# Kernel optimization log

Measured on AMD Instinct MI355X. Metric: run time of the kernel, lower is better.

Reference implementation:

```python
import jax, jax.numpy as jnp
import numpy as np

B, N, E, EMB, IN = 8192, 100, 1600, 5, 1
MLP_IN = 50 * 2 * EMB + 50 * 52  # 3100


def _glorot(k, shape):
    fan_in = shape[0]
    return (jax.random.normal(k, shape, jnp.float32) / np.sqrt(fan_in)).astype(jnp.float32)


def setup_inputs() -> dict:
    key = jax.random.key(0)
    ks = jax.random.split(key, 32)
    inp = {
        "data": jax.random.normal(ks[0], (B, N, IN), jnp.float32),
        "d": jax.random.normal(ks[1], (B, 50, 52), jnp.float32),
        "src": jax.random.randint(ks[2], (E,), 0, N, jnp.int32),
        "dst": jax.random.randint(ks[3], (E,), 0, N, jnp.int32),
    }
    # 3 GatedRGCN layers: (1->5), (5->5), (5->5); each has a feature linear W,b and a gate linear G,gb
    dims = [(IN, EMB), (EMB, EMB), (EMB, EMB)]
    for i, (fi, fo) in enumerate(dims):
        inp[f"W{i}"] = _glorot(ks[4 + 4 * i], (fi, fo))
        inp[f"b{i}"] = jnp.zeros((fo,), jnp.float32)
        inp[f"G{i}"] = _glorot(ks[5 + 4 * i], (fo, fo))
        inp[f"gb{i}"] = jnp.zeros((fo,), jnp.float32)
    # MLP head: 3100 -> 128 -> 128 -> 64 -> 2
    mdims = [(MLP_IN, 128), (128, 128), (128, 64), (64, 2)]
    for i, (fi, fo) in enumerate(mdims):
        inp[f"F{i + 1}"] = _glorot(ks[16 + 2 * i], (fi, fo))
        inp[f"fb{i + 1}"] = jnp.zeros((fo,), jnp.float32)
    return inp


def _gated_rgcn_layer(h, src, dst, W, b, G, gb):
    # h: [B, N, F_in]; sum-aggregate neighbor features along edges, then gated linear.
    msgs = h[:, src, :]                                   # [B, E, F_in] gather
    agg = jnp.zeros_like(h).at[:, dst, :].add(msgs)       # [B, N, F_in] scatter-add
    h2 = agg @ W + b                                      # [B, N, F_out]
    gate = jax.nn.sigmoid(h2 @ G + gb)                    # elementwise edge-free gate
    return jax.nn.leaky_relu(gate * h2)                   # LeakyReLU(0.01), torch default


def reference(data, d, src, dst,
              W0, b0, G0, gb0, W1, b1, G1, gb1, W2, b2, G2, gb2,
              F1, fb1, F2, fb2, F3, fb3, F4, fb4):
    x = data
    x = _gated_rgcn_layer(x, src, dst, W0, b0, G0, gb0)
    x = _gated_rgcn_layer(x, src, dst, W1, b1, G1, gb1)
    x = _gated_rgcn_layer(x, src, dst, W2, b2, G2, gb2)
    x = x.reshape(x.shape[0], -1)                         # [B, 500]
    x = jnp.concatenate([x, d.reshape(d.shape[0], -1)], axis=1)  # [B, 3100]
    x = jax.nn.leaky_relu(x @ F1 + fb1)
    x = jax.nn.leaky_relu(x @ F2 + fb2)
    x = jax.nn.leaky_relu(x @ F3 + fb3)
    x = jax.nn.sigmoid(x @ F4 + fb4)                      # [B, 2]
    return x
```

## Files before the change

kernel.cpp:

```cpp
#include <hip/hip_runtime.h>
#include <math.h>

#define NT 256
#define NTG 1024
constexpr int B_   = 8192;
constexpr int N_   = 100;
constexpr int E_   = 1600;
constexpr int EMB  = 5;
constexpr int XDIM = 500;
constexpr int DDIM = 2600;
constexpr int XWP  = 512;
constexpr int DOFF = 512;
constexpr int KPAD = 3136;
constexpr int NKC  = 98;
constexpr int H1 = 128, H2 = 128, H3 = 64, HO = 2;

typedef short short8 __attribute__((ext_vector_type(8)));
typedef float f32x4  __attribute__((ext_vector_type(4)));

__device__ __forceinline__ float leaky(float v) { return v > 0.f ? v : 0.01f * v; }
__device__ __forceinline__ float sigm(float v)  { return 1.f / (1.f + __expf(-v)); }
__device__ __forceinline__ unsigned short f2bf(float f) {
  unsigned int x = __float_as_uint(f);
  return (unsigned short)((x + 0x7fffu + ((x >> 16) & 1u)) >> 16);
}


constexpr int NDT = 6;

__global__ __launch_bounds__(NT) void setup_kernel(
    const int* __restrict__ src, const int* __restrict__ dst,
    int* __restrict__ off_g, int* __restrict__ lst_g,
    const float* __restrict__ F1, const float* __restrict__ F2, const float* __restrict__ F3,
    unsigned short* __restrict__ F1c, unsigned short* __restrict__ F2T, unsigned short* __restrict__ F3T,
    const float* __restrict__ dmat, unsigned short* __restrict__ awf)
{
  const int blk = blockIdx.x;
  const int t   = threadIdx.x;

  if (blk == 0) {
    __shared__ int cnt[N_ + 1];
    __shared__ int cur[N_];
    if (t <= N_) cnt[t] = 0;
    __syncthreads();
    for (int e = t; e < E_; e += NT) atomicAdd(&cnt[dst[e] + 1], 1);
    __syncthreads();
    if (t == 0) {
      int s = 0;
      for (int n = 0; n <= N_; ++n) { s += cnt[n]; cnt[n] = s; }
    }
    __syncthreads();
    if (t < N_) cur[t] = cnt[t];
    if (t <= N_) off_g[t] = cnt[t];
    __syncthreads();
    for (int e = t; e < E_; e += NT) {
      int d = dst[e];
      int p = atomicAdd(&cur[d], 1);
      lst_g[p] = src[e];
    }
  } else if (blk <= 320) {
    const int b = blk - 1;
    if (b < 128) {
      for (int k = t; k < KPAD; k += NT) {
        float v = 0.f;
        if (k < XDIM)                          v = F1[(size_t)k * H1 + b];
        else if (k >= DOFF && k < DOFF + DDIM) v = F1[(size_t)(k - DOFF + XDIM) * H1 + b];
        int kc = k >> 5, q = (k >> 3) & 3, e = k & 7;
        int lane = (b & 15) + q * 16;
        F1c[((size_t)(b >> 4) * NKC + kc) * 512 + lane * 8 + e] = f2bf(v);
      }
    } else if (b < 256) {
      int n = b - 128;
      if (t < 128) F2T[n * 128 + t] = f2bf(F2[(size_t)t * H2 + n]);
    } else {
      int n = b - 256;
      if (n < 64 && t < 128) F3T[n * 128 + t] = f2bf(F3[(size_t)t * H3 + n]);
    }
  } else {
    const int idx = blk - 321;
    const int R   = idx / NDT;
    const int ct  = idx - R * NDT;
    __shared__ __attribute__((aligned(16))) unsigned short tile[16][520];
    const float* dbase = dmat + (size_t)R * 16 * DDIM + ct * 512;

    if (ct < 5) {
      for (int i = t; i < 16 * 128; i += NT) {
        int r = i >> 7, c4 = i & 127;
        float4 f = *(const float4*)(dbase + (size_t)r * DDIM + c4 * 4);
        unsigned short* tp = &tile[r][c4 * 4];
        tp[0] = (unsigned short)(__float_as_uint(f.x) >> 16);
        tp[1] = (unsigned short)(__float_as_uint(f.y) >> 16);
        tp[2] = (unsigned short)(__float_as_uint(f.z) >> 16);
        tp[3] = (unsigned short)(__float_as_uint(f.w) >> 16);
      }
      __syncthreads();
      for (int i = t; i < 16 * 64; i += NT) {
        int kcL = i >> 6, lane = i & 63;
        int r = lane & 15, q = lane >> 4;
        uint4 p = *(const uint4*)&tile[r][kcL * 32 + q * 8];
        ((uint4*)awf)[((size_t)R * NKC + 16 + ct * 16 + kcL) * 64 + lane] = p;
      }
    } else {
      for (int i = t; i < 16 * 520; i += NT) ((unsigned short*)tile)[i] = 0;
      __syncthreads();
      for (int i = t; i < 16 * 10; i += NT) {
        int r = i / 10, c4 = i - r * 10;
        float4 f = *(const float4*)(dbase + (size_t)r * DDIM + c4 * 4);
        unsigned short* tp = &tile[r][c4 * 4];
        tp[0] = (unsigned short)(__float_as_uint(f.x) >> 16);
        tp[1] = (unsigned short)(__float_as_uint(f.y) >> 16);
        tp[2] = (unsigned short)(__float_as_uint(f.z) >> 16);
        tp[3] = (unsigned short)(__float_as_uint(f.w) >> 16);
      }
      __syncthreads();
      for (int i = t; i < 2 * 64; i += NT) {
        int kcL = i >> 6, lane = i & 63;
        int r = lane & 15, q = lane >> 4;
        uint4 p = *(const uint4*)&tile[r][kcL * 32 + q * 8];
        ((uint4*)awf)[((size_t)R * NKC + 96 + kcL) * 64 + lane] = p;
      }
    }
  }
}

constexpr int BT2 = 32;

__device__ __forceinline__ void rgcn_layer(
    const float* __restrict__ RB, float* __restrict__ WB,
    const float* __restrict__ wts, const int* __restrict__ soff,
    const int* __restrict__ sl160, int t, int wof)
{
  if (t < N_ * (BT2 / 4)) {
    const int n  = t >> 3;
    const int b4 = (t & 7) * 4;
    f32x4 a[5];
#pragma unroll
    for (int j = 0; j < 5; ++j) a[j] = (f32x4){0.f, 0.f, 0.f, 0.f};
    const int qe = soff[n + 1];
    for (int q = soff[n]; q < qe; ++q) {
      const float* base = RB + sl160[q] + b4;
#pragma unroll
      for (int j = 0; j < 5; ++j) a[j] += *(const f32x4*)(base + j * 32);
    }
    f32x4 h2[5];
#pragma unroll
    for (int j = 0; j < 5; ++j) {
      float bb = wts[wof + 25 + j];
      f32x4 v = (f32x4){bb, bb, bb, bb};
#pragma unroll
      for (int k = 0; k < 5; ++k) v += a[k] * wts[wof + k * 5 + j];
      h2[j] = v;
    }
#pragma unroll
    for (int j = 0; j < 5; ++j) {
      float gb = wts[wof + 55 + j];
      f32x4 g = (f32x4){gb, gb, gb, gb};
#pragma unroll
      for (int k = 0; k < 5; ++k) g += h2[k] * wts[wof + 30 + k * 5 + j];
      f32x4 o;
#pragma unroll
      for (int c = 0; c < 4; ++c) o[c] = leaky(sigm(g[c]) * h2[j][c]);
      *(f32x4*)(WB + n * 160 + j * 32 + b4) = o;
    }
  }
}

__global__ __launch_bounds__(NTG) void gnn_kernel(
    const float* __restrict__ data,
    const int* __restrict__ off_g, const int* __restrict__ lst_g,
    const float* __restrict__ W0, const float* __restrict__ b0, const float* __restrict__ G0, const float* __restrict__ gb0,
    const float* __restrict__ W1, const float* __restrict__ b1, const float* __restrict__ G1, const float* __restrict__ gb1,
    const float* __restrict__ W2, const float* __restrict__ b2, const float* __restrict__ G2, const float* __restrict__ gb2,
    unsigned short* __restrict__ awf)
{
  __shared__ __attribute__((aligned(16))) float bufA[BT2 * 513];
  __shared__ __attribute__((aligned(16))) float bufB[XDIM * BT2];
  __shared__ int   soff[N_ + 1];
  __shared__ int   sl160[E_];
  __shared__ float wts[160];
  const int t   = threadIdx.x;
  const int b0_ = blockIdx.x * BT2;

  for (int i = t; i < E_; i += NTG) sl160[i] = lst_g[i] * 160;
  if (t <= N_) soff[t] = off_g[t];
  if (t < 5)  { wts[t] = W0[t]; wts[5 + t] = b0[t]; wts[35 + t] = gb0[t]; }
  if (t < 25) { wts[10 + t] = G0[t];
                wts[40 + t] = W1[t]; wts[70 + t]  = G1[t];
                wts[100 + t] = W2[t]; wts[130 + t] = G2[t]; }
  if (t < 5)  { wts[65 + t] = b1[t]; wts[95 + t]  = gb1[t];
                wts[125 + t] = b2[t]; wts[155 + t] = gb2[t]; }
  for (int i = t; i < N_ * BT2; i += NTG) {
    int b = i / N_, n = i - b * N_;
    bufA[n * 160 + b] = data[(size_t)b0_ * N_ + i];
  }
  __syncthreads();

  if (t < N_ * (BT2 / 4)) {
    const int n  = t >> 3;
    const int b4 = (t & 7) * 4;
    f32x4 a = (f32x4){0.f, 0.f, 0.f, 0.f};
    const int qe = soff[n + 1];
    for (int q = soff[n]; q < qe; ++q) a += *(const f32x4*)(bufA + sl160[q] + b4);
    f32x4 h2[5];
#pragma unroll
    for (int j = 0; j < 5; ++j) {
      float bb = wts[5 + j];
      h2[j] = a * wts[j] + (f32x4){bb, bb, bb, bb};
    }
#pragma unroll
    for (int j = 0; j < 5; ++j) {
      float gb = wts[35 + j];
      f32x4 g = (f32x4){gb, gb, gb, gb};
#pragma unroll
      for (int k = 0; k < 5; ++k) g += h2[k] * wts[10 + k * 5 + j];
      f32x4 o;
#pragma unroll
      for (int c = 0; c < 4; ++c) o[c] = leaky(sigm(g[c]) * h2[j][c]);
      *(f32x4*)(bufB + n * 160 + j * 32 + b4) = o;
    }
  }
  __syncthreads();

  rgcn_layer(bufB, bufA, wts, soff, sl160, t, 40);
  __syncthreads();
  rgcn_layer(bufA, bufB, wts, soff, sl160, t, 100);
  __syncthreads();

  for (int i = t; i < BT2 * XWP; i += NTG) {
    int b = i & 31, r = i >> 5;
    bufA[b * 513 + r] = (r < XDIM) ? bufB[r * 32 + b] : 0.f;
  }
  __syncthreads();

  {
    const int R0 = blockIdx.x * 2;
    for (int i = t; i < 32 * 64; i += NTG) {
      int f = i >> 6, lane = i & 63;
      int h = f >> 4, kc = f & 15;
      int b = h * 16 + (lane & 15);
      int k0 = kc * 32 + (lane >> 4) * 8;
      const float* sp = bufA + b * 513 + k0;
      uint4 p;
      p.x = (unsigned)f2bf(sp[0]) | ((unsigned)f2bf(sp[1]) << 16);
      p.y = (unsigned)f2bf(sp[2]) | ((unsigned)f2bf(sp[3]) << 16);
      p.z = (unsigned)f2bf(sp[4]) | ((unsigned)f2bf(sp[5]) << 16);
      p.w = (unsigned)f2bf(sp[6]) | ((unsigned)f2bf(sp[7]) << 16);
      ((uint4*)awf)[((size_t)(R0 + h) * NKC + kc) * 64 + lane] = p;
    }
  }
}

constexpr int MBG = 32;
constexpr int MB2 = 16;
constexpr int EST = 136;
constexpr int KSPLIT = 7;
constexpr int SCC = 7;

__global__ __launch_bounds__(NT, 4) void mlp_main(
    const unsigned short* __restrict__ awf,
    const unsigned short* __restrict__ F1c, float* __restrict__ part)
{
  const int t     = threadIdx.x;
  const int rb    = blockIdx.x & 255;
  const int split = blockIdx.x >> 8;
  const int row0  = rb * MBG;
  const int lane  = t & 63;
  const int w     = t >> 6;
  const int quad  = lane >> 4;
  const int ln    = lane & 15;
  const int kc0   = split * (2 * SCC);

  const unsigned short* a0p = awf + (((size_t)(rb * 2 + 0) * NKC + kc0) * 64 + lane) * 8;
  const unsigned short* a1p = awf + (((size_t)(rb * 2 + 1) * NKC + kc0) * 64 + lane) * 8;
  const unsigned short* b0p = F1c + (((size_t)(w * 2 + 0) * NKC + kc0) * 64 + lane) * 8;
  const unsigned short* b1p = F1c + (((size_t)(w * 2 + 1) * NKC + kc0) * 64 + lane) * 8;

#define LOADF(Ax, Bx, c)                                                       \
  {                                                                            \
    _Pragma("unroll")                                                          \
    for (int s_ = 0; s_ < 2; ++s_) {                                           \
      const int o_ = (2 * (c) + s_) * 512;                                     \
      Ax[s_][0] = *(const short8*)(a0p + o_);                                  \
      Ax[s_][1] = *(const short8*)(a1p + o_);                                  \
      Bx[s_][0] = *(const short8*)(b0p + o_);                                  \
      Bx[s_][1] = *(const short8*)(b1p + o_);                                  \
    }                                                                          \
  }

  f32x4 a00 = {0.f, 0.f, 0.f, 0.f};
  f32x4 a01 = {0.f, 0.f, 0.f, 0.f};
  f32x4 a10 = {0.f, 0.f, 0.f, 0.f};
  f32x4 a11 = {0.f, 0.f, 0.f, 0.f};
  short8 A0[2][2], A1[2][2], B0[2][2], B1[2][2];

  LOADF(A0, B0, 0)
  LOADF(A1, B1, 1)
  for (int c = 0; c < SCC; ++c) {
    if (c & 1) {
#pragma unroll
      for (int s = 0; s < 2; ++s) {
        a00 = __builtin_amdgcn_mfma_f32_16x16x32_bf16(A1[s][0], B1[s][0], a00, 0, 0, 0);
        a01 = __builtin_amdgcn_mfma_f32_16x16x32_bf16(A1[s][0], B1[s][1], a01, 0, 0, 0);
        a10 = __builtin_amdgcn_mfma_f32_16x16x32_bf16(A1[s][1], B1[s][0], a10, 0, 0, 0);
        a11 = __builtin_amdgcn_mfma_f32_16x16x32_bf16(A1[s][1], B1[s][1], a11, 0, 0, 0);
      }
      if (c + 2 < SCC) LOADF(A1, B1, c + 2)
    } else {
#pragma unroll
      for (int s = 0; s < 2; ++s) {
        a00 = __builtin_amdgcn_mfma_f32_16x16x32_bf16(A0[s][0], B0[s][0], a00, 0, 0, 0);
        a01 = __builtin_amdgcn_mfma_f32_16x16x32_bf16(A0[s][0], B0[s][1], a01, 0, 0, 0);
        a10 = __builtin_amdgcn_mfma_f32_16x16x32_bf16(A0[s][1], B0[s][0], a10, 0, 0, 0);
        a11 = __builtin_amdgcn_mfma_f32_16x16x32_bf16(A0[s][1], B0[s][1], a11, 0, 0, 0);
      }
      if (c + 2 < SCC) LOADF(A0, B0, c + 2)
    }
  }
#undef LOADF

  const int col0 = w * 32 + ln;
  float* pp = part + ((size_t)split * B_ + row0) * H1;
#pragma unroll
  for (int r = 0; r < 4; ++r) {
    int m = quad * 4 + r;
    pp[m * H1 + col0]             = a00[r];
    pp[m * H1 + col0 + 16]        = a01[r];
    pp[(m + 16) * H1 + col0]      = a10[r];
    pp[(m + 16) * H1 + col0 + 16] = a11[r];
  }
}

__global__ __launch_bounds__(NT) void tail_kernel(
    const float* __restrict__ part, const float* __restrict__ fb1,
    const unsigned short* __restrict__ F2T, const float* __restrict__ fb2,
    const unsigned short* __restrict__ F3T, const float* __restrict__ fb3,
    const float* __restrict__ F4, const float* __restrict__ fb4,
    float* __restrict__ out)
{
  __shared__ __attribute__((aligned(16))) unsigned short sH[MB2 * EST];
  __shared__ float sh3[MB2 * 68];

  const int t    = threadIdx.x;
  const int row0 = blockIdx.x * MB2;
  const int lane = t & 63;
  const int w    = t >> 6;
  const int quad = lane >> 4;
  const int ln   = lane & 15;
  const int q8   = quad * 8;
  constexpr size_t PS = (size_t)B_ * H1;

  for (int i = t; i < MB2 * H1; i += NT) {
    int m = i >> 7, col = i & 127;
    size_t off = (size_t)(row0 + m) * H1 + col;
    float v = fb1[col];
#pragma unroll
    for (int s = 0; s < KSPLIT; ++s) v += part[s * PS + off];
    sH[m * EST + col] = f2bf(leaky(v));
  }
  __syncthreads();

  const int col0 = w * 32 + ln;
  f32x4 a20 = {0.f, 0.f, 0.f, 0.f};
  f32x4 a21 = {0.f, 0.f, 0.f, 0.f};
  {
    const unsigned short* g2a = F2T + (size_t)col0 * H2 + q8;
    const unsigned short* g2b = g2a + (size_t)16 * H2;
#pragma unroll
    for (int s = 0; s < 4; ++s) {
      short8 b0f = *(const short8*)(g2a + s * 32);
      short8 b1f = *(const short8*)(g2b + s * 32);
      short8 af  = *(const short8*)(sH + ln * EST + s * 32 + q8);
      a20 = __builtin_amdgcn_mfma_f32_16x16x32_bf16(af, b0f, a20, 0, 0, 0);
      a21 = __builtin_amdgcn_mfma_f32_16x16x32_bf16(af, b1f, a21, 0, 0, 0);
    }
  }
  __syncthreads();
  {
    float bb0 = fb2[col0], bb1 = fb2[col0 + 16];
#pragma unroll
    for (int r = 0; r < 4; ++r) {
      int m = quad * 4 + r;
      sH[m * EST + col0]      = f2bf(leaky(a20[r] + bb0));
      sH[m * EST + col0 + 16] = f2bf(leaky(a21[r] + bb1));
    }
  }
  __syncthreads();

  f32x4 a3 = {0.f, 0.f, 0.f, 0.f};
  {
    const unsigned short* g3 = F3T + (size_t)(w * 16 + ln) * H2 + q8;
#pragma unroll
    for (int s = 0; s < 4; ++s) {
      short8 bf = *(const short8*)(g3 + s * 32);
      short8 af = *(const short8*)(sH + ln * EST + s * 32 + q8);
      a3 = __builtin_amdgcn_mfma_f32_16x16x32_bf16(af, bf, a3, 0, 0, 0);
    }
  }
  {
    int col = w * 16 + ln;
    float bb = fb3[col];
#pragma unroll
    for (int r = 0; r < 4; ++r)
      sh3[(quad * 4 + r) * 68 + col] = leaky(a3[r] + bb);
  }
  __syncthreads();

  if (t < MB2 * HO) {
    int m = t >> 1, j = t & 1;
    float a = fb4[j];
#pragma unroll 8
    for (int k = 0; k < H3; ++k) a += sh3[m * 68 + k] * F4[k * HO + j];
    out[(size_t)(row0 + m) * HO + j] = sigm(a);
  }
}

extern "C" void kernel_launch(void* const* d_in, const int* in_sizes, int n_in,
                              void* d_out, int out_size, void* d_ws, size_t ws_size,
                              hipStream_t stream) {
  const float* data = (const float*)d_in[0];
  const float* dmat = (const float*)d_in[1];
  const int*   src  = (const int*)d_in[2];
  const int*   dst  = (const int*)d_in[3];
  const float* W0 = (const float*)d_in[4];  const float* b0 = (const float*)d_in[5];
  const float* G0 = (const float*)d_in[6];  const float* gb0 = (const float*)d_in[7];
  const float* W1 = (const float*)d_in[8];  const float* b1 = (const float*)d_in[9];
  const float* G1 = (const float*)d_in[10]; const float* gb1 = (const float*)d_in[11];
  const float* W2 = (const float*)d_in[12]; const float* b2 = (const float*)d_in[13];
  const float* G2 = (const float*)d_in[14]; const float* gb2 = (const float*)d_in[15];
  const float* F1 = (const float*)d_in[16]; const float* fb1 = (const float*)d_in[17];
  const float* F2 = (const float*)d_in[18]; const float* fb2 = (const float*)d_in[19];
  const float* F3 = (const float*)d_in[20]; const float* fb3 = (const float*)d_in[21];
  const float* F4 = (const float*)d_in[22]; const float* fb4 = (const float*)d_in[23];
  float* out = (float*)d_out;

  unsigned short* awf = (unsigned short*)d_ws;
  unsigned short* F1c = awf + (size_t)B_ * KPAD;
  unsigned short* F2T = F1c + 128 * KPAD;
  unsigned short* F3T = F2T + 128 * 128;
  int* off_g = (int*)(F3T + 64 * 128);
  int* lst_g = off_g + 104;
  float* part = (float*)(lst_g + 1600);

  setup_kernel<<<1 + 320 + 512 * NDT, NT, 0, stream>>>(src, dst, off_g, lst_g,
                                                       F1, F2, F3, F1c, F2T, F3T,
                                                       dmat, awf);
  gnn_kernel<<<B_ / BT2, NTG, 0, stream>>>(data, off_g, lst_g,
                                           W0, b0, G0, gb0,
                                           W1, b1, G1, gb1,
                                           W2, b2, G2, gb2, awf);
  mlp_main<<<(B_ / MBG) * KSPLIT, NT, 0, stream>>>(awf, F1c, part);
  tail_kernel<<<B_ / MB2, NT, 0, stream>>>(part, fb1, F2T, fb2,
                                           F3T, fb3, F4, fb4, out);
}
```

Before: 238.8 us.

## Fuse MLP tail into split-K kernel via last-block atomic counter

Removes the separate tail kernel launch: each split-K block of mlp_main increments a per-row-block counter, and the last of the seven splits to finish reduces the partials and runs layers 2-4 for its 32 rows in two 16-row halves. Counters are zeroed in setup_kernel. This saves one launch and its gap, but the tail work is now serialized in at most 256 blocks (one per row block) instead of 512 blocks, and it adds threadfences and extra LDS per block in mlp_main, which may affect occupancy.

```diff
diff --git a/kernel.cpp b/kernel.cpp
--- a/kernel.cpp
+++ b/kernel.cpp
@@ -30,7 +30,7 @@
 
 __global__ __launch_bounds__(NT) void setup_kernel(
     const int* __restrict__ src, const int* __restrict__ dst,
-    int* __restrict__ off_g, int* __restrict__ lst_g,
+    int* __restrict__ off_g, int* __restrict__ lst_g, int* __restrict__ cnt_g,
     const float* __restrict__ F1, const float* __restrict__ F2, const float* __restrict__ F3,
     unsigned short* __restrict__ F1c, unsigned short* __restrict__ F2T, unsigned short* __restrict__ F3T,
     const float* __restrict__ dmat, unsigned short* __restrict__ awf)
@@ -41,6 +41,7 @@
   if (blk == 0) {
     __shared__ int cnt[N_ + 1];
     __shared__ int cur[N_];
+    cnt_g[t] = 0;
     if (t <= N_) cnt[t] = 0;
     __syncthreads();
     for (int e = t; e < E_; e += NT) atomicAdd(&cnt[dst[e] + 1], 1);
@@ -251,15 +252,23 @@
 }
 
 constexpr int MBG = 32;
-constexpr int MB2 = 16;
 constexpr int EST = 136;
 constexpr int KSPLIT = 7;
 constexpr int SCC = 7;
 
 __global__ __launch_bounds__(NT, 4) void mlp_main(
     const unsigned short* __restrict__ awf,
-    const unsigned short* __restrict__ F1c, float* __restrict__ part)
+    const unsigned short* __restrict__ F1c, float* __restrict__ part,
+    int* __restrict__ cnt_g, const float* __restrict__ fb1,
+    const unsigned short* __restrict__ F2T, const float* __restrict__ fb2,
+    const unsigned short* __restrict__ F3T, const float* __restrict__ fb3,
+    const float* __restrict__ F4, const float* __restrict__ fb4,
+    float* __restrict__ out)
 {
+  __shared__ __attribute__((aligned(16))) unsigned short sH[16 * EST];
+  __shared__ float sh3[16 * 68];
+  __shared__ int isLast;
+
   const int t     = threadIdx.x;
   const int rb    = blockIdx.x & 255;
   const int split = blockIdx.x >> 8;
@@ -268,6 +277,7 @@
   const int w     = t >> 6;
   const int quad  = lane >> 4;
   const int ln    = lane & 15;
+  const int q8    = quad * 8;
   const int kc0   = split * (2 * SCC);
 
   const unsigned short* a0p = awf + (((size_t)(rb * 2 + 0) * NKC + kc0) * 64 + lane) * 8;
@@ -328,89 +338,82 @@
     pp[(m + 16) * H1 + col0]      = a10[r];
     pp[(m + 16) * H1 + col0 + 16] = a11[r];
   }
-}
-
-__global__ __launch_bounds__(NT) void tail_kernel(
-    const float* __restrict__ part, const float* __restrict__ fb1,
-    const unsigned short* __restrict__ F2T, const float* __restrict__ fb2,
-    const unsigned short* __restrict__ F3T, const float* __restrict__ fb3,
-    const float* __restrict__ F4, const float* __restrict__ fb4,
-    float* __restrict__ out)
-{
-  __shared__ __attribute__((aligned(16))) unsigned short sH[MB2 * EST];
-  __shared__ float sh3[MB2 * 68];
-
-  const int t    = threadIdx.x;
-  const int row0 = blockIdx.x * MB2;
-  const int lane = t & 63;
-  const int w    = t >> 6;
-  const int quad = lane >> 4;
-  const int ln   = lane & 15;
-  const int q8   = quad * 8;
+
+  if (t == 0) {
+    __threadfence();
+    int old = atomicAdd(&cnt_g[rb], 1);
+    isLast = (old == KSPLIT - 1);
+  }
+  __syncthreads();
+  if (!isLast) return;
+  __threadfence();
+
   constexpr size_t PS = (size_t)B_ * H1;
-
-  for (int i = t; i < MB2 * H1; i += NT) {
-    int m = i >> 7, col = i & 127;
-    size_t off = (size_t)(row0 + m) * H1 + col;
-    float v = fb1[col];
-#pragma unroll
-    for (int s = 0; s < KSPLIT; ++s) v += part[s * PS + off];
-    sH[m * EST + col] = f2bf(leaky(v));
-  }
-  __syncthreads();
-
-  const int col0 = w * 32 + ln;
-  f32x4 a20 = {0.f, 0.f, 0.f, 0.f};
-  f32x4 a21 = {0.f, 0.f, 0.f, 0.f};
-  {
-    const unsigned short* g2a = F2T + (size_t)col0 * H2 + q8;
-    const unsigned short* g2b = g2a + (size_t)16 * H2;
-#pragma unroll
-    for (int s = 0; s < 4; ++s) {
-      short8 b0f = *(const short8*)(g2a + s * 32);
-      short8 b1f = *(const short8*)(g2b + s * 32);
-      short8 af  = *(const short8*)(sH + ln * EST + s * 32 + q8);
-      a20 = __builtin_amdgcn_mfma_f32_16x16x32_bf16(af, b0f, a20, 0, 0, 0);
-      a21 = __builtin_amdgcn_mfma_f32_16x16x32_bf16(af, b1f, a21, 0, 0, 0);
-    }
-  }
-  __syncthreads();
-  {
-    float bb0 = fb2[col0], bb1 = fb2[col0 + 16];
-#pragma unroll
-    for (int r = 0; r < 4; ++r) {
-      int m = quad * 4 + r;
-      sH[m * EST + col0]      = f2bf(leaky(a20[r] + bb0));
-      sH[m * EST + col0 + 16] = f2bf(leaky(a21[r] + bb1));
-    }
-  }
-  __syncthreads();
-
-  f32x4 a3 = {0.f, 0.f, 0.f, 0.f};
-  {
-    const unsigned short* g3 = F3T + (size_t)(w * 16 + ln) * H2 + q8;
-#pragma unroll
-    for (int s = 0; s < 4; ++s) {
-      short8 bf = *(const short8*)(g3 + s * 32);
-      short8 af = *(const short8*)(sH + ln * EST + s * 32 + q8);
-      a3 = __builtin_amdgcn_mfma_f32_16x16x32_bf16(af, bf, a3, 0, 0, 0);
-    }
-  }
-  {
-    int col = w * 16 + ln;
-    float bb = fb3[col];
-#pragma unroll
-    for (int r = 0; r < 4; ++r)
-      sh3[(quad * 4 + r) * 68 + col] = leaky(a3[r] + bb);
-  }
-  __syncthreads();
-
-  if (t < MB2 * HO) {
-    int m = t >> 1, j = t & 1;
-    float a = fb4[j];
+  for (int hs = 0; hs < 2; ++hs) {
+    const int r0h = row0 + hs * 16;
+    for (int i = t; i < 16 * H1; i += NT) {
+      int m = i >> 7, col = i & 127;
+      size_t off = (size_t)(r0h + m) * H1 + col;
+      float v = fb1[col];
+#pragma unroll
+      for (int s = 0; s < KSPLIT; ++s) v += part[s * PS + off];
+      sH[m * EST + col] = f2bf(leaky(v));
+    }
+    __syncthreads();
+
+    f32x4 a20 = {0.f, 0.f, 0.f, 0.f};
+    f32x4 a21 = {0.f, 0.f, 0.f, 0.f};
+    {
+      const unsigned short* g2a = F2T + (size_t)col0 * H2 + q8;
+      const unsigned short* g2b = g2a + (size_t)16 * H2;
+#pragma unroll
+      for (int s = 0; s < 4; ++s) {
+        short8 b0f = *(const short8*)(g2a + s * 32);
+        short8 b1f = *(const short8*)(g2b + s * 32);
+        short8 af  = *(const short8*)(sH + ln * EST + s * 32 + q8);
+        a20 = __builtin_amdgcn_mfma_f32_16x16x32_bf16(af, b0f, a20, 0, 0, 0);
+        a21 = __builtin_amdgcn_mfma_f32_16x16x32_bf16(af, b1f, a21, 0, 0, 0);
+      }
+    }
+    __syncthreads();
+    {
+      float bb0 = fb2[col0], bb1 = fb2[col0 + 16];
+#pragma unroll
+      for (int r = 0; r < 4; ++r) {
+        int m = quad * 4 + r;
+        sH[m * EST + col0]      = f2bf(leaky(a20[r] + bb0));
+        sH[m * EST + col0 + 16] = f2bf(leaky(a21[r] + bb1));
+      }
+    }
+    __syncthreads();
+
+    f32x4 a3 = {0.f, 0.f, 0.f, 0.f};
+    {
+      const unsigned short* g3 = F3T + (size_t)(w * 16 + ln) * H2 + q8;
+#pragma unroll
+      for (int s = 0; s < 4; ++s) {
+        short8 bf = *(const short8*)(g3 + s * 32);
+        short8 af = *(const short8*)(sH + ln * EST + s * 32 + q8);
+        a3 = __builtin_amdgcn_mfma_f32_16x16x32_bf16(af, bf, a3, 0, 0, 0);
+      }
+    }
+    {
+      int col = w * 16 + ln;
+      float bb = fb3[col];
+#pragma unroll
+      for (int r = 0; r < 4; ++r)
+        sh3[(quad * 4 + r) * 68 + col] = leaky(a3[r] + bb);
+    }
+    __syncthreads();
+
+    if (t < 16 * HO) {
+      int m = t >> 1, j = t & 1;
+      float a = fb4[j];
 #pragma unroll 8
-    for (int k = 0; k < H3; ++k) a += sh3[m * 68 + k] * F4[k * HO + j];
-    out[(size_t)(row0 + m) * HO + j] = sigm(a);
+      for (int k = 0; k < H3; ++k) a += sh3[m * 68 + k] * F4[k * HO + j];
+      out[(size_t)(r0h + m) * HO + j] = sigm(a);
+    }
+    __syncthreads();
   }
 }
 
@@ -439,16 +442,17 @@
   unsigned short* F3T = F2T + 128 * 128;
   int* off_g = (int*)(F3T + 64 * 128);
   int* lst_g = off_g + 104;
-  float* part = (float*)(lst_g + 1600);
-
-  setup_kernel<<<1 + 320 + 512 * NDT, NT, 0, stream>>>(src, dst, off_g, lst_g,
+  int* cnt_g = lst_g + 1600;
+  float* part = (float*)(cnt_g + 256);
+
+  setup_kernel<<<1 + 320 + 512 * NDT, NT, 0, stream>>>(src, dst, off_g, lst_g, cnt_g,
                                                        F1, F2, F3, F1c, F2T, F3T,
                                                        dmat, awf);
   gnn_kernel<<<B_ / BT2, NTG, 0, stream>>>(data, off_g, lst_g,
                                            W0, b0, G0, gb0,
                                            W1, b1, G1, gb1,
                                            W2, b2, G2, gb2, awf);
-  mlp_main<<<(B_ / MBG) * KSPLIT, NT, 0, stream>>>(awf, F1c, part);
-  tail_kernel<<<B_ / MB2, NT, 0, stream>>>(part, fb1, F2T, fb2,
-                                           F3T, fb3, F4, fb4, out);
-}
+  mlp_main<<<(B_ / MBG) * KSPLIT, NT, 0, stream>>>(awf, F1c, part, cnt_g,
+                                                   fb1, F2T, fb2,
+                                                   F3T, fb3, F4, fb4, out);
+}
```

After: 384.8 us. 1.61x slower.
